# Kernel tuning notes

Measured on AMD Instinct MI355X. Metric: run time of the kernel, lower is better.

Reference implementation:

```python
import jax, jax.numpy as jnp
import numpy as np

EPS = 1e-9
N, E = 100000, 1000000
IN_F, OUT_F, HEADS = 128, 64, 2


def normalize_points(x):
    # UHG projective normalize: unit-norm spatial part, keep last (homogeneous) coord
    n = jnp.linalg.norm(x[..., :-1], axis=-1, keepdims=True)
    return jnp.concatenate([x[..., :-1] / jnp.maximum(n, EPS), x[..., -1:]], axis=-1)


def uhg_inner(a, b):
    # hyperbolic inner product: spatial dot minus time-time product
    return jnp.sum(a[..., :-1] * b[..., :-1], axis=-1) - a[..., -1] * b[..., -1]


def compute_cross_ratio(p1, p2, p3, p4):
    num = uhg_inner(p1, p3) * uhg_inner(p2, p4)
    den = uhg_inner(p1, p4) * uhg_inner(p2, p3)
    return num / jnp.where(jnp.abs(den) < EPS, EPS, den)


def restore_cross_ratio(x, cr_target):
    cr_cur = compute_cross_ratio(x[0], x[1], x[2], x[3])
    scale = jnp.abs(cr_target / jnp.where(jnp.abs(cr_cur) < EPS, EPS, cr_cur)) ** 0.25
    return x * scale


def setup_inputs() -> dict:
    key = jax.random.key(0)
    ks = jax.random.split(key, 10)
    s_in = 1.0 / np.sqrt(IN_F)
    s_hid = 1.0 / np.sqrt(OUT_F * HEADS)
    H = OUT_F * HEADS
    return {
        "x": jax.random.normal(ks[0], (N, IN_F), dtype=jnp.float32),
        "edge_index": jax.random.randint(ks[1], (2, E), 0, N, dtype=jnp.int64),
        "Wq": jax.random.uniform(ks[2], (H, IN_F), jnp.float32, -s_in, s_in),
        "bq": jnp.zeros((H,), jnp.float32),
        "Wk": jax.random.uniform(ks[3], (H, IN_F), jnp.float32, -s_in, s_in),
        "bk": jnp.zeros((H,), jnp.float32),
        "Wv": jax.random.uniform(ks[4], (H, IN_F), jnp.float32, -s_in, s_in),
        "bv": jnp.zeros((H,), jnp.float32),
        "Wo": jax.random.uniform(ks[5], (OUT_F, H), jnp.float32, -s_hid, s_hid),
        "bo": jnp.zeros((OUT_F,), jnp.float32),
    }


def reference(x, edge_index, Wq, bq, Wk, bk, Wv, bv, Wo, bo):
    n = x.shape[0]
    cr_initial = compute_cross_ratio(x[0], x[1], x[2], x[3])
    x_proj = normalize_points(x)
    q = (x_proj @ Wq.T + bq).reshape(n, HEADS, OUT_F)
    k = (x_proj @ Wk.T + bk).reshape(n, HEADS, OUT_F)
    v = (x_proj @ Wv.T + bv).reshape(n, HEADS, OUT_F)
    row, col = edge_index[0], edge_index[1]
    qe = normalize_points(q[row])  # [E, H, D]
    ke = normalize_points(k[col])
    scores = uhg_inner(qe, ke) / np.sqrt(IN_F)  # [E, H]
    alpha = jax.nn.softmax(scores, axis=0)  # global softmax over edges (as in source)
    msgs = v[col] * alpha[..., None]  # [E, H, D]
    out = jax.ops.segment_sum(msgs, row, num_segments=n)  # [N, H, D]
    out = out.reshape(n, HEADS * OUT_F)
    out = out @ Wo.T + bo
    out = restore_cross_ratio(out, cr_initial)
    return out
```

## Files before the change

kernel.cpp:

```cpp
#include <hip/hip_runtime.h>
#include <math.h>

#define EPSF 1e-9f
#define INV_SQRT128 0.08838834764831845f

typedef _Float16 half8 __attribute__((ext_vector_type(8)));
typedef float f32x4 __attribute__((ext_vector_type(4)));

__device__ __forceinline__ void gl_lds16(const void* g, void* l) {
    __builtin_amdgcn_global_load_lds((const __attribute__((address_space(1))) void*)g,
                                     (__attribute__((address_space(3))) void*)l, 16, 0, 0);
}

__global__ void k_wpack(const float* __restrict__ Wq, const float* __restrict__ Wk,
                        const float* __restrict__ Wv, half8* __restrict__ whi,
                        half8* __restrict__ wlo, float* __restrict__ w127) {
    int t = blockIdx.x * 256 + threadIdx.x;
    if (t >= 6144) return;
    int col = t & 127, g = (t >> 7) & 3, ks = (t >> 9) & 3, kind = t >> 11;
    const float* W = (kind == 0) ? Wq : (kind == 1) ? Wk : Wv;
    const float4* W4 = (const float4*)W;
    float4 a = W4[col * 32 + ks * 8 + g * 2];
    float4 b = W4[col * 32 + ks * 8 + g * 2 + 1];
    float xv[8] = {a.x, a.y, a.z, a.w, b.x, b.y, b.z, b.w};
    half8 h, lo;
#pragma unroll
    for (int j = 0; j < 8; j++) {
        _Float16 hh = (_Float16)xv[j];
        h[j] = hh;
        lo[j] = (_Float16)((xv[j] - (float)hh) * 4096.0f);
    }
    whi[t] = h;
    wlo[t] = lo;
    if (ks == 3 && g == 3) w127[kind * 128 + col] = xv[7];
}

__global__ void k_wpack2(const float* __restrict__ Wo, half8* __restrict__ wohi,
                         half8* __restrict__ wolo) {
    int t = blockIdx.x * 256 + threadIdx.x;
    if (t >= 1024) return;
    int col = t & 63, g = (t >> 6) & 3, ks = t >> 8;
    const float4* W4 = (const float4*)Wo;
    float4 a = W4[col * 32 + ks * 8 + g * 2];
    float4 b = W4[col * 32 + ks * 8 + g * 2 + 1];
    float xv[8] = {a.x, a.y, a.z, a.w, b.x, b.y, b.z, b.w};
    half8 h, lo;
#pragma unroll
    for (int j = 0; j < 8; j++) {
        _Float16 hh = (_Float16)xv[j];
        h[j] = hh;
        lo[j] = (_Float16)((xv[j] - (float)hh) * 4096.0f);
    }
    wohi[t] = h;
    wolo[t] = lo;
}

__global__ void __launch_bounds__(256, 2)
k_qkvm(const float* __restrict__ x,
       const half8* __restrict__ whi, const half8* __restrict__ wlo,
       const float* __restrict__ w127,
       const float* __restrict__ bq, const float* __restrict__ bk,
       const float* __restrict__ bv,
       float* __restrict__ qn, float* __restrict__ kn, float* __restrict__ vn,
       const int* __restrict__ ei, int* __restrict__ bcnt,
       int N, int E, int chunk) {
    int b = (int)blockIdx.x;
    __shared__ half8 bsh[4096];
    if (b < 512 && (b & 1)) {
        int* h = (int*)bsh;
        int t = threadIdx.x;
        int hid = b >> 1;
        h[t] = 0;
        __syncthreads();
        int s = hid * chunk, e1 = min(s + chunk, E);
        for (int e = s + t; e < e1; e += 256) atomicAdd(&h[ei[e] >> 9], 1);
        __syncthreads();
        bcnt[hid * 256 + t] = h[t];
        return;
    }
    int gb = (b < 512) ? (b >> 1) : (b - 256);

    int tid = threadIdx.x;
    int wv = tid >> 6;
    int l = tid & 63;
    int r = l & 15;
    int g = l >> 4;
    int rowbase = gb * 128 + wv * 32;
    const float4* x4 = (const float4*)x;

    {
        const half8* sH = whi + wv * 512;
        const half8* sL = wlo + wv * 512;
#pragma unroll
        for (int i = 0; i < 8; i++) {
            gl_lds16(sH + i * 64 + l, bsh + wv * 512 + i * 64);
            gl_lds16(sL + i * 64 + l, bsh + 2048 + wv * 512 + i * 64);
        }
    }

    half8 hiA[2][4], loA[2][4];
    float rnj[2][4], tcj[2][4];
#pragma unroll
    for (int t = 0; t < 2; t++) {
        int row = min(rowbase + t * 16 + r, N - 1);
        float ssum = 0.f, tl = 0.f;
#pragma unroll
        for (int ks = 0; ks < 4; ks++) {
            float4 a = x4[(size_t)row * 32 + ks * 8 + g * 2];
            float4 bb = x4[(size_t)row * 32 + ks * 8 + g * 2 + 1];
            float xv[8] = {a.x, a.y, a.z, a.w, bb.x, bb.y, bb.z, bb.w};
#pragma unroll
            for (int j = 0; j < 8; j++) {
                _Float16 hh = (_Float16)xv[j];
                hiA[t][ks][j] = hh;
                loA[t][ks][j] = (_Float16)((xv[j] - (float)hh) * 4096.0f);
                ssum += xv[j] * xv[j];
            }
            if (ks == 3 && g == 3) { tl = xv[7]; ssum -= xv[7] * xv[7]; }
        }
        ssum += __shfl_xor(ssum, 16);
        ssum += __shfl_xor(ssum, 32);
        float rn = 1.f / fmaxf(sqrtf(ssum), EPSF);
        float tla = __shfl(tl, 48 + r);
        float tc = tla * (1.f - rn);
#pragma unroll
        for (int j = 0; j < 4; j++) {
            rnj[t][j] = __shfl(rn, g * 4 + j);
            tcj[t][j] = __shfl(tc, g * 4 + j);
        }
    }

    asm volatile("s_waitcnt vmcnt(0)" ::: "memory");
    __syncthreads();

    const float* const bks[3] = {bq, bk, bv};
    bool lane15 = (r == 15);
    const f32x4 zz = {0.f, 0.f, 0.f, 0.f};
    int dsbase = g * 128 + r;

    for (int kind = 0; kind < 3; kind++) {
        float wcA[2][4], bbA[2][4];
#pragma unroll
        for (int h = 0; h < 2; h++)
#pragma unroll
            for (int ct = 0; ct < 4; ct++) {
                int col = (h * 4 + ct) * 16 + r;
                wcA[h][ct] = w127[kind * 128 + col];
                bbA[h][ct] = bks[kind][col];
            }

#pragma unroll
        for (int h = 0; h < 2; h++) {
            f32x4 aM[2][4], aX[2][4];
#pragma unroll
            for (int t = 0; t < 2; t++)
#pragma unroll
                for (int ct = 0; ct < 4; ct++) { aM[t][ct] = zz; aX[t][ct] = zz; }

#pragma unroll
            for (int ks = 0; ks < 4; ks++) {
                half8 hB[4], lB[4];
#pragma unroll
                for (int ct = 0; ct < 4; ct++) {
                    int bi = dsbase + ks * 512 + (h * 4 + ct) * 16;
                    hB[ct] = bsh[bi];
                    lB[ct] = bsh[2048 + bi];
                }
#pragma unroll
                for (int ct = 0; ct < 4; ct++) {
                    aM[0][ct] = __builtin_amdgcn_mfma_f32_16x16x32_f16(hiA[0][ks], hB[ct], aM[0][ct], 0, 0, 0);
                    aM[1][ct] = __builtin_amdgcn_mfma_f32_16x16x32_f16(hiA[1][ks], hB[ct], aM[1][ct], 0, 0, 0);
                    aX[0][ct] = __builtin_amdgcn_mfma_f32_16x16x32_f16(hiA[0][ks], lB[ct], aX[0][ct], 0, 0, 0);
                    aX[0][ct] = __builtin_amdgcn_mfma_f32_16x16x32_f16(loA[0][ks], hB[ct], aX[0][ct], 0, 0, 0);
                    aX[1][ct] = __builtin_amdgcn_mfma_f32_16x16x32_f16(hiA[1][ks], lB[ct], aX[1][ct], 0, 0, 0);
                    aX[1][ct] = __builtin_amdgcn_mfma_f32_16x16x32_f16(loA[1][ks], hB[ct], aX[1][ct], 0, 0, 0);
                }
            }

#pragma unroll
            for (int t = 0; t < 2; t++) {
                float cv[4][4];
#pragma unroll
                for (int ct = 0; ct < 4; ct++)
#pragma unroll
                    for (int j = 0; j < 4; j++) {
                        float acc = aM[t][ct][j] + aX[t][ct][j] * (1.0f / 4096.0f);
                        cv[ct][j] = fmaf(rnj[t][j], acc, fmaf(tcj[t][j], wcA[h][ct], bbA[h][ct]));
                    }
                if (kind < 2) {
#pragma unroll
                    for (int j = 0; j < 4; j++) {
                        float ss = 0.f;
#pragma unroll
                        for (int ct = 0; ct < 4; ct++) {
                            float c = cv[ct][j];
                            ss += (ct == 3 && lane15) ? 0.f : c * c;
                        }
                        ss += __shfl_xor(ss, 1);
                        ss += __shfl_xor(ss, 2);
                        ss += __shfl_xor(ss, 4);
                        ss += __shfl_xor(ss, 8);
                        float rh = 1.f / fmaxf(sqrtf(ss), EPSF);
#pragma unroll
                        for (int ct = 0; ct < 4; ct++) {
                            bool ist = (ct == 3) && lane15;
                            if (!ist) cv[ct][j] *= rh;
                            if (kind == 0) {
                                if (ist) cv[ct][j] = -cv[ct][j];
                                cv[ct][j] *= INV_SQRT128;
                            }
                        }
                    }
                }
#pragma unroll
                for (int j = 0; j < 4; j++) {
                    int row = rowbase + t * 16 + g * 4 + j;
                    if (row < N) {
                        float* dst = (kind == 0) ? qn : (kind == 1 ? kn : vn);
                        dst += (size_t)row * 128;
#pragma unroll
                        for (int ct = 0; ct < 4; ct++)
                            dst[(h * 4 + ct) * 16 + r] = cv[ct][j];
                    }
                }
            }
        }

        if (kind < 2) {
            __syncthreads();
            const half8* sH = whi + (kind + 1) * 2048 + wv * 512;
            const half8* sL = wlo + (kind + 1) * 2048 + wv * 512;
#pragma unroll
            for (int i = 0; i < 8; i++) {
                gl_lds16(sH + i * 64 + l, bsh + wv * 512 + i * 64);
                gl_lds16(sL + i * 64 + l, bsh + 2048 + wv * 512 + i * 64);
            }
            asm volatile("s_waitcnt vmcnt(0)" ::: "memory");
            __syncthreads();
        }
    }
}

__global__ void k_bin2(int* __restrict__ bcnt, int* __restrict__ bintot) {
    __shared__ int sd[256];
    int b = blockIdx.x, t = threadIdx.x;
    int v = bcnt[t * 256 + b];
    sd[t] = v;
    __syncthreads();
    for (int off = 1; off < 256; off <<= 1) {
        int val = sd[t];
        int add = (t >= off) ? sd[t - off] : 0;
        __syncthreads();
        sd[t] = val + add;
        __syncthreads();
    }
    bcnt[t * 256 + b] = sd[t] - v;
    if (t == 255) bintot[b] = sd[255];
}

__global__ void k_bin3(const int* __restrict__ bintot, int* __restrict__ binoff,
                       int* __restrict__ offs, int N, int E) {
    __shared__ int sd[256];
    int t = threadIdx.x;
    int v = bintot[t];
    sd[t] = v;
    __syncthreads();
    for (int off = 1; off < 256; off <<= 1) {
        int val = sd[t];
        int add = (t >= off) ? sd[t - off] : 0;
        __syncthreads();
        sd[t] = val + add;
        __syncthreads();
    }
    binoff[t] = sd[t] - v;
    if (t == 255) {
        binoff[256] = sd[255];
        offs[N] = E;
    }
}

__global__ void k_scat1(const int* __restrict__ ei, const int* __restrict__ bcnt,
                        const int* __restrict__ binoff, int* __restrict__ packed,
                        int E, int chunk) {
    __shared__ int cur[256];
    int t = threadIdx.x, b = blockIdx.x;
    cur[t] = binoff[t] + bcnt[b * 256 + t];
    __syncthreads();
    int s = b * chunk, e1 = min(s + chunk, E);
    for (int e = s + t; e < e1; e += 256) {
        int r = ei[e];
        int c = ei[E + e];
        int p = atomicAdd(&cur[r >> 9], 1);
        packed[p] = ((r & 511) << 17) | c;
    }
}

__global__ void __launch_bounds__(256)
k_sortf(const int* __restrict__ packed, const int* __restrict__ binoff,
        int* __restrict__ ccol, int* __restrict__ offs, int N) {
    __shared__ int seg[6656];
    __shared__ int h[512];
    __shared__ int sc[256];
    int b = blockIdx.x, t = threadIdx.x;
    int s = binoff[b], e1 = binoff[b + 1];
    int cnt = min(e1 - s, 6656);
    for (int i = t; i < cnt; i += 256) seg[i] = packed[s + i];
    h[t] = 0;
    h[t + 256] = 0;
    __syncthreads();
    for (int i = t; i < cnt; i += 256) atomicAdd(&h[seg[i] >> 17], 1);
    __syncthreads();
    int v0 = h[2 * t], v1 = h[2 * t + 1];
    int pair = v0 + v1;
    sc[t] = pair;
    __syncthreads();
    for (int off = 1; off < 256; off <<= 1) {
        int val = sc[t];
        int add = (t >= off) ? sc[t - off] : 0;
        __syncthreads();
        sc[t] = val + add;
        __syncthreads();
    }
    int pexcl = sc[t] - pair;
    __syncthreads();
    h[2 * t] = pexcl;
    h[2 * t + 1] = pexcl + v0;
    int rowbase = b << 9;
    if (rowbase + 2 * t < N) offs[rowbase + 2 * t] = s + h[2 * t];
    if (rowbase + 2 * t + 1 < N) offs[rowbase + 2 * t + 1] = s + h[2 * t + 1];
    __syncthreads();
    for (int i = t; i < cnt; i += 256) {
        int pk = seg[i];
        int p = atomicAdd(&h[pk >> 17], 1);
        ccol[s + p] = pk & 0x1FFFF;
    }
}

__global__ void k_score(const float* __restrict__ qn, const float* __restrict__ kn,
                        const int* __restrict__ offs, const int* __restrict__ ccol,
                        float* __restrict__ e2, double* __restrict__ psum, int N, int E) {
    int g = threadIdx.x >> 5;
    int l = threadIdx.x & 31;
    int head = l >> 4;
    int n = blockIdx.x * 8 + g;
    double esum = 0.0;
    if (n < N) {
        float4 q4 = ((const float4*)qn)[(size_t)n * 32 + l];
        int s0 = offs[n], s1 = offs[n + 1];
        const float4* k4p = (const float4*)kn;
        float* eh = e2 + (size_t)head * E;
        int i = s0;
        for (; i + 4 <= s1; i += 4) {
            int c0 = ccol[i];
            int c1 = ccol[i + 1];
            int c2 = ccol[i + 2];
            int c3 = ccol[i + 3];
            float4 ka = k4p[(size_t)c0 * 32 + l];
            float4 kb = k4p[(size_t)c1 * 32 + l];
            float4 kc = k4p[(size_t)c2 * 32 + l];
            float4 kd = k4p[(size_t)c3 * 32 + l];
            float p0 = q4.x * ka.x;
            p0 = fmaf(q4.y, ka.y, p0); p0 = fmaf(q4.z, ka.z, p0); p0 = fmaf(q4.w, ka.w, p0);
            float p1 = q4.x * kb.x;
            p1 = fmaf(q4.y, kb.y, p1); p1 = fmaf(q4.z, kb.z, p1); p1 = fmaf(q4.w, kb.w, p1);
            float p2 = q4.x * kc.x;
            p2 = fmaf(q4.y, kc.y, p2); p2 = fmaf(q4.z, kc.z, p2); p2 = fmaf(q4.w, kc.w, p2);
            float p3 = q4.x * kd.x;
            p3 = fmaf(q4.y, kd.y, p3); p3 = fmaf(q4.z, kd.z, p3); p3 = fmaf(q4.w, kd.w, p3);
            p0 += __shfl_xor(p0, 1); p1 += __shfl_xor(p1, 1);
            p2 += __shfl_xor(p2, 1); p3 += __shfl_xor(p3, 1);
            p0 += __shfl_xor(p0, 2); p1 += __shfl_xor(p1, 2);
            p2 += __shfl_xor(p2, 2); p3 += __shfl_xor(p3, 2);
            p0 += __shfl_xor(p0, 4); p1 += __shfl_xor(p1, 4);
            p2 += __shfl_xor(p2, 4); p3 += __shfl_xor(p3, 4);
            p0 += __shfl_xor(p0, 8); p1 += __shfl_xor(p1, 8);
            p2 += __shfl_xor(p2, 8); p3 += __shfl_xor(p3, 8);
            float x0 = expf(p0);
            float x1 = expf(p1);
            float x2 = expf(p2);
            float x3 = expf(p3);
            if ((l & 15) == 0) {
                eh[i] = x0;
                eh[i + 1] = x1;
                eh[i + 2] = x2;
                eh[i + 3] = x3;
                esum += (double)((x0 + x1) + (x2 + x3));
            }
        }
        for (; i < s1; i++) {
            int c = ccol[i];
            float4 k4 = k4p[(size_t)c * 32 + l];
            float p = q4.x * k4.x;
            p = fmaf(q4.y, k4.y, p); p = fmaf(q4.z, k4.z, p); p = fmaf(q4.w, k4.w, p);
            p += __shfl_xor(p, 1);
            p += __shfl_xor(p, 2);
            p += __shfl_xor(p, 4);
            p += __shfl_xor(p, 8);
            float x = expf(p);
            if ((l & 15) == 0) {
                eh[i] = x;
                esum += (double)x;
            }
        }
    }
    __shared__ double sd[2][8];
    if ((l & 15) == 0) sd[head][g] = esum;
    __syncthreads();
    if (threadIdx.x < 2) {
        double s = 0.0;
        for (int i2 = 0; i2 < 8; i2++) s += sd[threadIdx.x][i2];
        psum[(size_t)blockIdx.x * 2 + threadIdx.x] = s;
    }
}

__global__ void k_aggr(const float* __restrict__ vn, const int* __restrict__ offs,
                       const int* __restrict__ ccol, const float* __restrict__ e2,
                       float* __restrict__ U, int N, int E) {
    int g = threadIdx.x >> 5;
    int l = threadIdx.x & 31;
    int head = l >> 4;
    int n = blockIdx.x * 8 + g;
    if (n >= N) return;
    int s0 = offs[n], s1 = offs[n + 1];
    const float4* v4p = (const float4*)vn;
    const float* eh = e2 + (size_t)head * E;
    float4 acc = {0.f, 0.f, 0.f, 0.f};
    int i = s0;
    for (; i + 4 <= s1; i += 4) {
        int c0 = ccol[i];
        int c1 = ccol[i + 1];
        int c2 = ccol[i + 2];
        int c3 = ccol[i + 3];
        float4 va = v4p[(size_t)c0 * 32 + l];
        float4 vb = v4p[(size_t)c1 * 32 + l];
        float4 vc = v4p[(size_t)c2 * 32 + l];
        float4 vd = v4p[(size_t)c3 * 32 + l];
        float x0 = eh[i];
        float x1 = eh[i + 1];
        float x2 = eh[i + 2];
        float x3 = eh[i + 3];
        acc.x = fmaf(va.x, x0, acc.x); acc.y = fmaf(va.y, x0, acc.y);
        acc.z = fmaf(va.z, x0, acc.z); acc.w = fmaf(va.w, x0, acc.w);
        acc.x = fmaf(vb.x, x1, acc.x); acc.y = fmaf(vb.y, x1, acc.y);
        acc.z = fmaf(vb.z, x1, acc.z); acc.w = fmaf(vb.w, x1, acc.w);
        acc.x = fmaf(vc.x, x2, acc.x); acc.y = fmaf(vc.y, x2, acc.y);
        acc.z = fmaf(vc.z, x2, acc.z); acc.w = fmaf(vc.w, x2, acc.w);
        acc.x = fmaf(vd.x, x3, acc.x); acc.y = fmaf(vd.y, x3, acc.y);
        acc.z = fmaf(vd.z, x3, acc.z); acc.w = fmaf(vd.w, x3, acc.w);
    }
    for (; i < s1; i++) {
        int c = ccol[i];
        float4 v4 = v4p[(size_t)c * 32 + l];
        float x = eh[i];
        acc.x = fmaf(v4.x, x, acc.x); acc.y = fmaf(v4.y, x, acc.y);
        acc.z = fmaf(v4.z, x, acc.z); acc.w = fmaf(v4.w, x, acc.w);
    }
    ((float4*)U)[(size_t)n * 32 + l] = acc;
}

__global__ void k_crout4(const float* __restrict__ x, const float* __restrict__ U,
                         const float* __restrict__ Wo, const float* __restrict__ bo,
                         const double* __restrict__ psum, int P,
                         double* __restrict__ sumf, float* __restrict__ scalef) {
    __shared__ float xs[4 * 128];
    __shared__ float o4[4 * 64];
    __shared__ double crin_sh;
    __shared__ double sdr[2][4];
    int tid = threadIdx.x;
    {
        double s0 = 0.0, s1 = 0.0;
        for (int i = tid; i < P; i += 256) {
            s0 += psum[2 * i];
            s1 += psum[2 * i + 1];
        }
        for (int off = 32; off; off >>= 1) {
            s0 += __shfl_xor(s0, off);
            s1 += __shfl_xor(s1, off);
        }
        int w = tid >> 6;
        if ((tid & 63) == 0) { sdr[0][w] = s0; sdr[1][w] = s1; }
    }
    xs[tid] = U[tid];
    xs[tid + 256] = U[tid + 256];
    __syncthreads();
    if (tid == 0) {
        double s0 = sdr[0][0] + sdr[0][1] + sdr[0][2] + sdr[0][3];
        double s1 = sdr[1][0] + sdr[1][1] + sdr[1][2] + sdr[1][3];
        sumf[0] = s0;
        sumf[1] = s1;
    }
    if (tid >= 64 && tid < 128) {
        int l = tid - 64;
        const int pa[4] = {0, 1, 0, 1};
        const int pb[4] = {2, 3, 3, 2};
        double inner[4];
        for (int p = 0; p < 4; p++) {
            const float* a = x + pa[p] * 128;
            const float* b = x + pb[p] * 128;
            double s = (double)a[l] * (double)b[l];
            double t = (double)a[l + 64] * (double)b[l + 64];
            s += (l == 63) ? -t : t;
            for (int off = 32; off; off >>= 1) s += __shfl_xor(s, off);
            inner[p] = s;
        }
        if (l == 0) {
            double num = inner[0] * inner[1];
            double den = inner[2] * inner[3];
            if (fabs(den) < 1e-9) den = 1e-9;
            crin_sh = num / den;
        }
    }
    __syncthreads();
    int w = tid >> 6, o = tid & 63;
    float si0 = (float)(1.0 / sumf[0]);
    float si1 = (float)(1.0 / sumf[1]);
    const float* xr = xs + w * 128;
    const float* wr = Wo + (size_t)o * 128;
    float d0 = 0.f, d1 = 0.f;
    for (int j = 0; j < 64; j++) d0 = fmaf(xr[j], wr[j], d0);
    for (int j = 64; j < 128; j++) d1 = fmaf(xr[j], wr[j], d1);
    o4[w * 64 + o] = d0 * si0 + d1 * si1 + bo[o];
    __syncthreads();
    if (tid < 64) {
        int l = tid;
        const int pa[4] = {0, 1, 0, 1};
        const int pb[4] = {2, 3, 3, 2};
        double inner[4];
        for (int p = 0; p < 4; p++) {
            double t = (double)o4[pa[p] * 64 + l] * (double)o4[pb[p] * 64 + l];
            if (l == 63) t = -t;
            for (int off = 32; off; off >>= 1) t += __shfl_xor(t, off);
            inner[p] = t;
        }
        if (l == 0) {
            double num = inner[0] * inner[1];
            double den = inner[2] * inner[3];
            if (fabs(den) < 1e-9) den = 1e-9;
            double crc = num / den;
            if (fabs(crc) < 1e-9) crc = 1e-9;
            double ratio = crin_sh / crc;
            scalef[0] = (float)pow(fabs(ratio), 0.25);
        }
    }
}

__global__ void __launch_bounds__(256, 2)
k_outm(const float* __restrict__ U, const half8* __restrict__ wohi,
       const half8* __restrict__ wolo, const float* __restrict__ bo,
       const double* __restrict__ sumf, const float* __restrict__ scalef,
       float* __restrict__ out, int N) {
    __shared__ half8 bsh[2048];
    int tid = threadIdx.x;
    int wv = tid >> 6;
    int l = tid & 63;
    int r = l & 15;
    int g = l >> 4;
    int rowbase = blockIdx.x * 128 + wv * 32;

    {
        const half8* sH = wohi + wv * 256;
        const half8* sL = wolo + wv * 256;
#pragma unroll
        for (int i = 0; i < 4; i++) {
            gl_lds16(sH + i * 64 + l, bsh + wv * 256 + i * 64);
            gl_lds16(sL + i * 64 + l, bsh + 1024 + wv * 256 + i * 64);
        }
    }

    float si0 = (float)(1.0 / sumf[0]);
    float si1 = (float)(1.0 / sumf[1]);
    const float4* U4 = (const float4*)U;
    half8 hiA[2][4], loA[2][4];
#pragma unroll
    for (int t = 0; t < 2; t++) {
        int row = min(rowbase + t * 16 + r, N - 1);
#pragma unroll
        for (int ks = 0; ks < 4; ks++) {
            float si = (ks < 2) ? si0 : si1;
            float4 a = U4[(size_t)row * 32 + ks * 8 + g * 2];
            float4 b = U4[(size_t)row * 32 + ks * 8 + g * 2 + 1];
            float xv[8] = {a.x, a.y, a.z, a.w, b.x, b.y, b.z, b.w};
#pragma unroll
            for (int j = 0; j < 8; j++) {
                float v = xv[j] * si;
                _Float16 hh = (_Float16)v;
                hiA[t][ks][j] = hh;
                loA[t][ks][j] = (_Float16)((v - (float)hh) * 4096.0f);
            }
        }
    }

    asm volatile("s_waitcnt vmcnt(0)" ::: "memory");
    __syncthreads();

    const f32x4 zz = {0.f, 0.f, 0.f, 0.f};
    f32x4 aM[2][4], aX[2][4];
#pragma unroll
    for (int t = 0; t < 2; t++)
#pragma unroll
        for (int ct = 0; ct < 4; ct++) { aM[t][ct] = zz; aX[t][ct] = zz; }

#pragma unroll
    for (int ks = 0; ks < 4; ks++) {
        half8 hB[4], lB[4];
#pragma unroll
        for (int ct = 0; ct < 4; ct++) {
            int bi = ks * 256 + g * 64 + ct * 16 + r;
            hB[ct] = bsh[bi];
            lB[ct] = bsh[1024 + bi];
        }
#pragma unroll
        for (int ct = 0; ct < 4; ct++) {
            aM[0][ct] = __builtin_amdgcn_mfma_f32_16x16x32_f16(hiA[0][ks], hB[ct], aM[0][ct], 0, 0, 0);
            aM[1][ct] = __builtin_amdgcn_mfma_f32_16x16x32_f16(hiA[1][ks], hB[ct], aM[1][ct], 0, 0, 0);
            aX[0][ct] = __builtin_amdgcn_mfma_f32_16x16x32_f16(hiA[0][ks], lB[ct], aX[0][ct], 0, 0, 0);
            aX[0][ct] = __builtin_amdgcn_mfma_f32_16x16x32_f16(loA[0][ks], hB[ct], aX[0][ct], 0, 0, 0);
            aX[1][ct] = __builtin_amdgcn_mfma_f32_16x16x32_f16(hiA[1][ks], lB[ct], aX[1][ct], 0, 0, 0);
            aX[1][ct] = __builtin_amdgcn_mfma_f32_16x16x32_f16(loA[1][ks], hB[ct], aX[1][ct], 0, 0, 0);
        }
    }

    float sf = scalef[0];
#pragma unroll
    for (int t = 0; t < 2; t++)
#pragma unroll
        for (int ct = 0; ct < 4; ct++) {
            float bb = bo[ct * 16 + r];
#pragma unroll
            for (int j = 0; j < 4; j++) {
                int row = rowbase + t * 16 + g * 4 + j;
                if (row < N) {
                    float c = (aM[t][ct][j] + aX[t][ct][j] * (1.0f / 4096.0f) + bb) * sf;
                    out[(size_t)row * 64 + ct * 16 + r] = c;
                }
            }
        }
}

extern "C" void kernel_launch(void* const* d_in, const int* in_sizes, int n_in,
                              void* d_out, int out_size, void* d_ws, size_t ws_size,
                              hipStream_t stream) {
    const float* x  = (const float*)d_in[0];
    const int*   ei = (const int*)d_in[1];
    const float* Wq = (const float*)d_in[2];
    const float* bq = (const float*)d_in[3];
    const float* Wk = (const float*)d_in[4];
    const float* bk = (const float*)d_in[5];
    const float* Wv = (const float*)d_in[6];
    const float* bv = (const float*)d_in[7];
    const float* Wo = (const float*)d_in[8];
    const float* bo = (const float*)d_in[9];
    float* out = (float*)d_out;

    const int N = in_sizes[0] / 128;
    const int E = in_sizes[1] / 2;
    const size_t NR = (size_t)N * 128;
    const int NGB = (N + 127) / 128;
    const int GB = (N + 7) / 8;
    const int chunk = (E + 255) / 256;
    const int NBINS = (N + 511) >> 9;

    float* qn = (float*)d_ws;
    float* kn = qn + NR;
    float* vn = kn + NR;
    int* offs = (int*)(vn + NR);
    int* ccol = offs + N + 2;
    int* bcnt = ccol + E;
    int* bintot = bcnt + 256 * 256;
    int* binoff = bintot + 256;
    uintptr_t pe = ((uintptr_t)(binoff + 257 + 1) + 15) & ~(uintptr_t)15;
    float* e2 = (float*)pe;
    uintptr_t pd = ((uintptr_t)(e2 + 2 * (size_t)E) + 7) & ~(uintptr_t)7;
    double* psum = (double*)pd;
    double* sumf = psum + (size_t)GB * 2;
    float* scalef = (float*)(sumf + 2);

    uintptr_t pw = ((uintptr_t)ccol + 15) & ~(uintptr_t)15;
    half8* whi = (half8*)pw;
    half8* wlo = whi + 6144;
    float* w127 = (float*)(wlo + 6144);

    uintptr_t pw2 = ((uintptr_t)bcnt + 15) & ~(uintptr_t)15;
    half8* wohi = (half8*)pw2;
    half8* wolo = wohi + 1024;

    float* U = qn;

    k_wpack<<<24, 256, 0, stream>>>(Wq, Wk, Wv, whi, wlo, w127);
    k_qkvm<<<NGB + 256, 256, 0, stream>>>(x, whi, wlo, w127, bq, bk, bv,
                                          qn, kn, vn, ei, bcnt, N, E, chunk);
    k_bin2<<<256, 256, 0, stream>>>(bcnt, bintot);
    k_bin3<<<1, 256, 0, stream>>>(bintot, binoff, offs, N, E);
    k_scat1<<<256, 256, 0, stream>>>(ei, bcnt, binoff, ccol, E, chunk);
    k_wpack2<<<4, 256, 0, stream>>>(Wo, wohi, wolo);
    k_sortf<<<NBINS, 256, 0, stream>>>(ccol, binoff, ccol, offs, N);
    k_score<<<GB, 256, 0, stream>>>(qn, kn, offs, ccol, e2, psum, N, E);
    k_aggr<<<GB, 256, 0, stream>>>(vn, offs, ccol, e2, U, N, E);
    k_crout4<<<1, 256, 0, stream>>>(x, U, Wo, bo, psum, GB, sumf, scalef);
    k_outm<<<NGB, 256, 0, stream>>>(U, wohi, wolo, bo, sumf, scalef, out, N);
}
```

Baseline: 406.7 us.

## Store normalized keys in fp16 and prefetch next weights during epilogue

```diff
diff --git a/kernel.cpp b/kernel.cpp
--- a/kernel.cpp
+++ b/kernel.cpp
@@ -5,6 +5,7 @@
 #define INV_SQRT128 0.08838834764831845f
 
 typedef _Float16 half8 __attribute__((ext_vector_type(8)));
+typedef _Float16 half4v __attribute__((ext_vector_type(4)));
 typedef float f32x4 __attribute__((ext_vector_type(4)));
 
 __device__ __forceinline__ void gl_lds16(const void* g, void* l) {
@@ -61,7 +62,7 @@
        const float* __restrict__ w127,
        const float* __restrict__ bq, const float* __restrict__ bk,
        const float* __restrict__ bv,
-       float* __restrict__ qn, float* __restrict__ kn, float* __restrict__ vn,
+       float* __restrict__ qn, _Float16* __restrict__ knh, float* __restrict__ vn,
        const int* __restrict__ ei, int* __restrict__ bcnt,
        int N, int E, int chunk) {
     int b = (int)blockIdx.x;
@@ -138,6 +139,7 @@
     const f32x4 zz = {0.f, 0.f, 0.f, 0.f};
     int dsbase = g * 128 + r;
 
+#pragma unroll
     for (int kind = 0; kind < 3; kind++) {
         float wcA[2][4], bbA[2][4];
 #pragma unroll
@@ -174,6 +176,17 @@
                     aX[0][ct] = __builtin_amdgcn_mfma_f32_16x16x32_f16(loA[0][ks], hB[ct], aX[0][ct], 0, 0, 0);
                     aX[1][ct] = __builtin_amdgcn_mfma_f32_16x16x32_f16(hiA[1][ks], lB[ct], aX[1][ct], 0, 0, 0);
                     aX[1][ct] = __builtin_amdgcn_mfma_f32_16x16x32_f16(loA[1][ks], hB[ct], aX[1][ct], 0, 0, 0);
+                }
+            }
+
+            if (h == 1 && kind < 2) {
+                __syncthreads();
+                const half8* sH = whi + (kind + 1) * 2048 + wv * 512;
+                const half8* sL = wlo + (kind + 1) * 2048 + wv * 512;
+#pragma unroll
+                for (int i = 0; i < 8; i++) {
+                    gl_lds16(sH + i * 64 + l, bsh + wv * 512 + i * 64);
+                    gl_lds16(sL + i * 64 + l, bsh + 2048 + wv * 512 + i * 64);
                 }
             }
 
@@ -216,25 +229,28 @@
                 for (int j = 0; j < 4; j++) {
                     int row = rowbase + t * 16 + g * 4 + j;
                     if (row < N) {
-                        float* dst = (kind == 0) ? qn : (kind == 1 ? kn : vn);
-                        dst += (size_t)row * 128;
-#pragma unroll
-                        for (int ct = 0; ct < 4; ct++)
-                            dst[(h * 4 + ct) * 16 + r] = cv[ct][j];
+                        if (kind == 0) {
+                            float* dst = qn + (size_t)row * 128;
+#pragma unroll
+                            for (int ct = 0; ct < 4; ct++)
+                                dst[(h * 4 + ct) * 16 + r] = cv[ct][j];
+                        } else if (kind == 1) {
+                            _Float16* dst = knh + (size_t)row * 128;
+#pragma unroll
+                            for (int ct = 0; ct < 4; ct++)
+                                dst[(h * 4 + ct) * 16 + r] = (_Float16)cv[ct][j];
+                        } else {
+                            float* dst = vn + (size_t)row * 128;
+#pragma unroll
+                            for (int ct = 0; ct < 4; ct++)
+                                dst[(h * 4 + ct) * 16 + r] = cv[ct][j];
+                        }
                     }
                 }
             }
         }
 
         if (kind < 2) {
-            __syncthreads();
-            const half8* sH = whi + (kind + 1) * 2048 + wv * 512;
-            const half8* sL = wlo + (kind + 1) * 2048 + wv * 512;
-#pragma unroll
-            for (int i = 0; i < 8; i++) {
-                gl_lds16(sH + i * 64 + l, bsh + wv * 512 + i * 64);
-                gl_lds16(sL + i * 64 + l, bsh + 2048 + wv * 512 + i * 64);
-            }
             asm volatile("s_waitcnt vmcnt(0)" ::: "memory");
             __syncthreads();
         }
@@ -336,7 +352,7 @@
     }
 }
 
-__global__ void k_score(const float* __restrict__ qn, const float* __restrict__ kn,
+__global__ void k_score(const float* __restrict__ qn, const _Float16* __restrict__ knh,
                         const int* __restrict__ offs, const int* __restrict__ ccol,
                         float* __restrict__ e2, double* __restrict__ psum, int N, int E) {
     int g = threadIdx.x >> 5;
@@ -347,7 +363,7 @@
     if (n < N) {
         float4 q4 = ((const float4*)qn)[(size_t)n * 32 + l];
         int s0 = offs[n], s1 = offs[n + 1];
-        const float4* k4p = (const float4*)kn;
+        const half4v* k4p = (const half4v*)knh;
         float* eh = e2 + (size_t)head * E;
         int i = s0;
         for (; i + 4 <= s1; i += 4) {
@@ -355,18 +371,22 @@
             int c1 = ccol[i + 1];
             int c2 = ccol[i + 2];
             int c3 = ccol[i + 3];
-            float4 ka = k4p[(size_t)c0 * 32 + l];
-            float4 kb = k4p[(size_t)c1 * 32 + l];
-            float4 kc = k4p[(size_t)c2 * 32 + l];
-            float4 kd = k4p[(size_t)c3 * 32 + l];
-            float p0 = q4.x * ka.x;
-            p0 = fmaf(q4.y, ka.y, p0); p0 = fmaf(q4.z, ka.z, p0); p0 = fmaf(q4.w, ka.w, p0);
-            float p1 = q4.x * kb.x;
-            p1 = fmaf(q4.y, kb.y, p1); p1 = fmaf(q4.z, kb.z, p1); p1 = fmaf(q4.w, kb.w, p1);
-            float p2 = q4.x * kc.x;
-            p2 = fmaf(q4.y, kc.y, p2); p2 = fmaf(q4.z, kc.z, p2); p2 = fmaf(q4.w, kc.w, p2);
-            float p3 = q4.x * kd.x;
-            p3 = fmaf(q4.y, kd.y, p3); p3 = fmaf(q4.z, kd.z, p3); p3 = fmaf(q4.w, kd.w, p3);
+            half4v ka = k4p[(size_t)c0 * 32 + l];
+            half4v kb = k4p[(size_t)c1 * 32 + l];
+            half4v kc = k4p[(size_t)c2 * 32 + l];
+            half4v kd = k4p[(size_t)c3 * 32 + l];
+            float p0 = q4.x * (float)ka[0];
+            p0 = fmaf(q4.y, (float)ka[1], p0); p0 = fmaf(q4.z, (float)ka[2], p0);
+            p0 = fmaf(q4.w, (float)ka[3], p0);
+            float p1 = q4.x * (float)kb[0];
+            p1 = fmaf(q4.y, (float)kb[1], p1); p1 = fmaf(q4.z, (float)kb[2], p1);
+            p1 = fmaf(q4.w, (float)kb[3], p1);
+            float p2 = q4.x * (float)kc[0];
+            p2 = fmaf(q4.y, (float)kc[1], p2); p2 = fmaf(q4.z, (float)kc[2], p2);
+            p2 = fmaf(q4.w, (float)kc[3], p2);
+            float p3 = q4.x * (float)kd[0];
+            p3 = fmaf(q4.y, (float)kd[1], p3); p3 = fmaf(q4.z, (float)kd[2], p3);
+            p3 = fmaf(q4.w, (float)kd[3], p3);
             p0 += __shfl_xor(p0, 1); p1 += __shfl_xor(p1, 1);
             p2 += __shfl_xor(p2, 1); p3 += __shfl_xor(p3, 1);
             p0 += __shfl_xor(p0, 2); p1 += __shfl_xor(p1, 2);
@@ -389,17 +409,18 @@
         }
         for (; i < s1; i++) {
             int c = ccol[i];
-            float4 k4 = k4p[(size_t)c * 32 + l];
-            float p = q4.x * k4.x;
-            p = fmaf(q4.y, k4.y, p); p = fmaf(q4.z, k4.z, p); p = fmaf(q4.w, k4.w, p);
+            half4v k4 = k4p[(size_t)c * 32 + l];
+            float p = q4.x * (float)k4[0];
+            p = fmaf(q4.y, (float)k4[1], p); p = fmaf(q4.z, (float)k4[2], p);
+            p = fmaf(q4.w, (float)k4[3], p);
             p += __shfl_xor(p, 1);
             p += __shfl_xor(p, 2);
             p += __shfl_xor(p, 4);
             p += __shfl_xor(p, 8);
-            float x = expf(p);
+            float xx = expf(p);
             if ((l & 15) == 0) {
-                eh[i] = x;
-                esum += (double)x;
+                eh[i] = xx;
+                esum += (double)xx;
             }
         }
     }
@@ -451,9 +472,9 @@
     for (; i < s1; i++) {
         int c = ccol[i];
         float4 v4 = v4p[(size_t)c * 32 + l];
-        float x = eh[i];
-        acc.x = fmaf(v4.x, x, acc.x); acc.y = fmaf(v4.y, x, acc.y);
-        acc.z = fmaf(v4.z, x, acc.z); acc.w = fmaf(v4.w, x, acc.w);
+        float xx = eh[i];
+        acc.x = fmaf(v4.x, xx, acc.x); acc.y = fmaf(v4.y, xx, acc.y);
+        acc.z = fmaf(v4.z, xx, acc.z); acc.w = fmaf(v4.w, xx, acc.w);
     }
     ((float4*)U)[(size_t)n * 32 + l] = acc;
 }
@@ -661,9 +682,9 @@
     const int NBINS = (N + 511) >> 9;
 
     float* qn = (float*)d_ws;
-    float* kn = qn + NR;
-    float* vn = kn + NR;
-    int* offs = (int*)(vn + NR);
+    float* vn = qn + NR;
+    _Float16* knh = (_Float16*)(vn + NR);
+    int* offs = (int*)(knh + NR);
     int* ccol = offs + N + 2;
     int* bcnt = ccol + E;
     int* bintot = bcnt + 256 * 256;
@@ -688,13 +709,13 @@
 
     k_wpack<<<24, 256, 0, stream>>>(Wq, Wk, Wv, whi, wlo, w127);
     k_qkvm<<<NGB + 256, 256, 0, stream>>>(x, whi, wlo, w127, bq, bk, bv,
-                                          qn, kn, vn, ei, bcnt, N, E, chunk);
+                                          qn, knh, vn, ei, bcnt, N, E, chunk);
     k_bin2<<<256, 256, 0, stream>>>(bcnt, bintot);
     k_bin3<<<1, 256, 0, stream>>>(bintot, binoff, offs, N, E);
     k_scat1<<<256, 256, 0, stream>>>(ei, bcnt, binoff, ccol, E, chunk);
     k_wpack2<<<4, 256, 0, stream>>>(Wo, wohi, wolo);
     k_sortf<<<NBINS, 256, 0, stream>>>(ccol, binoff, ccol, offs, N);
-    k_score<<<GB, 256, 0, stream>>>(qn, kn, offs, ccol, e2, psum, N, E);
+    k_score<<<GB, 256, 0, stream>>>(qn, knh, offs, ccol, e2, psum, N, E);
     k_aggr<<<GB, 256, 0, stream>>>(vn, offs, ccol, e2, U, N, E);
     k_crout4<<<1, 256, 0, stream>>>(x, U, Wo, bo, psum, GB, sumf, scalef);
     k_outm<<<NGB, 256, 0, stream>>>(U, wohi, wolo, bo, sumf, scalef, out, N);
```

Result: faster. 382.1 us (-6.0%).
